# Kernel optimization log

Hardware: AMD Instinct MI355X
Metric: run time of the kernel (lower is better)

The kernel has to match this reference:

```python
import jax, jax.numpy as jnp
import numpy as np


def setup_inputs() -> dict:
    key = jax.random.key(0)
    kq, kk, kv = jax.random.split(key, 3)
    B, Q, K, D = 8, 2048, 2048, 1024
    return {
        "queries": jax.random.normal(kq, (B, Q, D), dtype=jnp.float32),
        "keys": jax.random.normal(kk, (B, K, D), dtype=jnp.float32),
        "values": jax.random.normal(kv, (B, K, D), dtype=jnp.float32),
    }


def reference(queries, keys, values):
    # scores: [B, Q, K] = queries @ keys^T
    scores = jnp.einsum("bqd,bkd->bqk", queries, keys)
    # NOTE: softmax over dim=1, i.e. the QUERY axis (non-standard)
    attn = jax.nn.softmax(scores, axis=1)
    # output: [B, Q, D]
    return jnp.einsum("bqk,bkd->bqd", attn, values)
```

## Files before the change

kernel.cpp:

```cpp
#include <hip/hip_runtime.h>
#include <stdint.h>

typedef _Float16 half8 __attribute__((ext_vector_type(8)));
typedef __attribute__((ext_vector_type(4))) float f32x4;
typedef __attribute__((ext_vector_type(8))) unsigned short us8;

__device__ inline unsigned short f2h(float x) {
  _Float16 h = (_Float16)x;
  return __builtin_bit_cast(unsigned short, h);
}

__device__ inline void ld16(const unsigned short* g, unsigned short* l) {
  __builtin_amdgcn_global_load_lds(
      (const __attribute__((address_space(1))) unsigned int*)g,
      (__attribute__((address_space(3))) unsigned int*)l, 16, 0, 0);
}

__global__ void k_cast16(const float* __restrict__ in, unsigned short* __restrict__ o, long n8) {
  long i = (long)blockIdx.x * blockDim.x + threadIdx.x;
  if (i >= n8) return;
  float4 a = ((const float4*)in)[i * 2];
  float4 b = ((const float4*)in)[i * 2 + 1];
  us8 h;
  h[0] = f2h(a.x); h[1] = f2h(a.y); h[2] = f2h(a.z); h[3] = f2h(a.w);
  h[4] = f2h(b.x); h[5] = f2h(b.y); h[6] = f2h(b.z); h[7] = f2h(b.w);
  *(us8*)(o + i * 8) = h;
}

__global__ void k_transpose16(const float* __restrict__ V, unsigned short* __restrict__ VT,
                              int Kn, int Dn) {
  __shared__ unsigned short t[64][65];
  const int b = blockIdx.z;
  const int k0 = blockIdx.x * 64, d0 = blockIdx.y * 64;
  const int c = threadIdx.x & 63, rr = threadIdx.x >> 6;
  const float* pV = V + (long)b * Kn * Dn;
  unsigned short* pT = VT + (long)b * Dn * Kn;
#pragma unroll
  for (int i = 0; i < 16; ++i) {
    int r = rr + i * 4;
    t[r][c] = f2h(pV[(long)(k0 + r) * Dn + d0 + c]);
  }
  __syncthreads();
#pragma unroll
  for (int i = 0; i < 16; ++i) {
    int r = rr + i * 4;
    pT[(long)(d0 + r) * Kn + k0 + c] = t[c][r];
  }
}


#define SBAR() __builtin_amdgcn_s_barrier()
#define SCHED0() __builtin_amdgcn_sched_barrier(0)
#define VMC(n) do { asm volatile("s_waitcnt vmcnt(" #n ")" ::: "memory"); } while (0)

template <int STATS>
__launch_bounds__(512, 2)
__global__ void k_gemm_bt(const unsigned short* __restrict__ A,
                          const unsigned short* __restrict__ B,
                          float* __restrict__ C, float2* __restrict__ ps,
                          int N, int Kin, long sA, long sB, long sC) {
  __shared__ unsigned short sAb[4][256 * 32];
  __shared__ unsigned short sBb[4][256 * 32];

  const int tid = threadIdx.x;
  const int lane = tid & 63, wave = tid >> 6;
  const int wr = wave >> 2, wc = wave & 3;
  const int l15 = lane & 15;

  const int nx = gridDim.x, ny = gridDim.y;
  int wg = ((int)blockIdx.z * ny + blockIdx.y) * nx + blockIdx.x;
  const int nwg = nx * ny * (int)gridDim.z;
  wg = (wg & 7) * (nwg >> 3) + (wg >> 3);
  const int tn = wg % nx, tm = (wg / nx) % ny, b = wg / (nx * ny);

  const unsigned short* pA = A + b * sA + (long)tm * 256 * Kin;
  const unsigned short* pB = B + b * sB + (long)tn * 256 * Kin;
  float* pC = C + b * sC;

  const int rlo = tid >> 2;
  const int csw = ((tid & 3) * 8) ^ (((rlo >> 1) & 3) << 3);
  const long ga = (long)rlo * Kin + csw;
  const long gh = (long)128 * Kin;

  const int ksw = ((lane >> 4) * 8) ^ (((l15 >> 1) & 3) << 3);
  const int aoff = (wr * 128 + l15) * 32 + ksw;
  const int boff = (wc * 64 + l15) * 32 + ksw;

#define STG(t, q) do { \
    ld16(pA + ga + (long)(t) * 32, &sAb[q][tid * 8]); \
    ld16(pA + ga + gh + (long)(t) * 32, &sAb[q][4096 + tid * 8]); \
    ld16(pB + ga + (long)(t) * 32, &sBb[q][tid * 8]); \
    ld16(pB + ga + gh + (long)(t) * 32, &sBb[q][4096 + tid * 8]); } while (0)

#define LDA8(q, m) (*(const half8*)&sAb[q][aoff + (m) * 512])
#define LDB8(q, n) (*(const half8*)&sBb[q][boff + (n) * 512])

  f32x4 acc[8][4];
#pragma unroll
  for (int i = 0; i < 8; ++i)
#pragma unroll
    for (int j = 0; j < 4; ++j)
#pragma unroll
      for (int r = 0; r < 4; ++r) acc[i][j][r] = 0.f;

  half8 aL[2][4], bC[2][4], aH[4];

#define READ_LO(s, q) \
  aL[s][0] = LDA8(q, 0); aL[s][1] = LDA8(q, 1); aL[s][2] = LDA8(q, 2); aL[s][3] = LDA8(q, 3); \
  bC[s][0] = LDB8(q, 0); bC[s][1] = LDB8(q, 1); bC[s][2] = LDB8(q, 2); bC[s][3] = LDB8(q, 3);

#define READ_HI(q) \
  aH[0] = LDA8(q, 4); aH[1] = LDA8(q, 5); aH[2] = LDA8(q, 6); aH[3] = LDA8(q, 7);

#define MFMA_ROW(m, a, s) \
  acc[m][0] = __builtin_amdgcn_mfma_f32_16x16x32_f16(a, bC[s][0], acc[m][0], 0, 0, 0); \
  acc[m][1] = __builtin_amdgcn_mfma_f32_16x16x32_f16(a, bC[s][1], acc[m][1], 0, 0, 0); \
  acc[m][2] = __builtin_amdgcn_mfma_f32_16x16x32_f16(a, bC[s][2], acc[m][2], 0, 0, 0); \
  acc[m][3] = __builtin_amdgcn_mfma_f32_16x16x32_f16(a, bC[s][3], acc[m][3], 0, 0, 0);

#define MFMA_LO(s) \
  __builtin_amdgcn_s_setprio(1); \
  MFMA_ROW(0, aL[s][0], s) MFMA_ROW(1, aL[s][1], s) \
  MFMA_ROW(2, aL[s][2], s) MFMA_ROW(3, aL[s][3], s) \
  __builtin_amdgcn_s_setprio(0);

#define MFMA_HI(s) \
  __builtin_amdgcn_s_setprio(1); \
  MFMA_ROW(4, aH[0], s) MFMA_ROW(5, aH[1], s) \
  MFMA_ROW(6, aH[2], s) MFMA_ROW(7, aH[3], s) \
  __builtin_amdgcn_s_setprio(0);

#define TILE_MAIN(t, s, sn) \
  READ_HI((t) & 3); \
  STG((t) + 2, ((t) + 2) & 3); \
  MFMA_LO(s) \
  VMC(4); SBAR(); SCHED0(); \
  READ_LO(sn, ((t) + 1) & 3); \
  MFMA_HI(s)

  const int nt = Kin >> 5;

  STG(0, 0);
  STG(1, 1);
  VMC(4); SBAR(); SCHED0();
  READ_LO(0, 0);

  for (int t = 0; t + 3 < nt; t += 2) {
    TILE_MAIN(t, 0, 1);
    TILE_MAIN(t + 1, 1, 0);
  }
  {
    READ_HI((nt - 2) & 3);
    MFMA_LO(0)
    VMC(0); SBAR(); SCHED0();
    READ_LO(1, (nt - 1) & 3);
    MFMA_HI(0)
    READ_HI((nt - 1) & 3);
    MFMA_LO(1)
    MFMA_HI(1)
  }

  const int crow0 = tm * 256 + wr * 128 + (lane >> 4) * 4;
  const int ccol0 = tn * 256 + wc * 64 + l15;
#pragma unroll
  for (int m = 0; m < 8; ++m)
#pragma unroll
    for (int n = 0; n < 4; ++n)
#pragma unroll
      for (int r = 0; r < 4; ++r)
        pC[(long)(crow0 + m * 16 + r) * N + ccol0 + n * 16] = acc[m][n][r];

  if constexpr (STATS) {
#pragma unroll
    for (int n = 0; n < 4; ++n) {
      float mx = -3.0e38f;
#pragma unroll
      for (int m = 0; m < 8; ++m)
#pragma unroll
        for (int r = 0; r < 4; ++r) mx = fmaxf(mx, acc[m][n][r]);
      mx = fmaxf(mx, __shfl_xor(mx, 16, 64));
      mx = fmaxf(mx, __shfl_xor(mx, 32, 64));
      float l = 0.f;
#pragma unroll
      for (int m = 0; m < 8; ++m)
#pragma unroll
        for (int r = 0; r < 4; ++r) l += __expf(acc[m][n][r] - mx);
      l += __shfl_xor(l, 16, 64);
      l += __shfl_xor(l, 32, 64);
      if (lane < 16) {
        int col = tn * 256 + wc * 64 + n * 16 + lane;
        ps[((long)(b * 16 + tm * 2 + wr)) * N + col] = make_float2(mx, l);
      }
    }
  }
}

__global__ void k_stats_combine(const float2* __restrict__ ps, float2* __restrict__ st, int Kn) {
  const long i = (long)blockIdx.x * blockDim.x + threadIdx.x;
  const int b = (int)(i / Kn), k = (int)(i % Kn);
  float M = -3.0e38f;
#pragma unroll
  for (int j = 0; j < 16; ++j) M = fmaxf(M, ps[((long)(b * 16 + j)) * Kn + k].x);
  float L = 0.f;
#pragma unroll
  for (int j = 0; j < 16; ++j) {
    float2 v = ps[((long)(b * 16 + j)) * Kn + k];
    L += v.y * __expf(v.x - M);
  }
  st[i] = make_float2(M, 1.0f / L);
}

__global__ void k_pcomp(const float* __restrict__ S, const float2* __restrict__ st,
                        unsigned short* __restrict__ P) {
  const long i = (long)blockIdx.x * blockDim.x + threadIdx.x;
  const long r = i >> 8;
  const int kb = (int)(i & 255) * 8;
  const int b = (int)(r >> 11);
  const float* sp = S + r * 2048 + kb;
  float4 s0 = *(const float4*)sp;
  float4 s1 = *(const float4*)(sp + 4);
  const float2* tp = st + (long)b * 2048 + kb;
  us8 o;
  float sv[8] = {s0.x, s0.y, s0.z, s0.w, s1.x, s1.y, s1.z, s1.w};
#pragma unroll
  for (int j = 0; j < 8; ++j) {
    float2 t = tp[j];
    o[j] = f2h(__expf(sv[j] - t.x) * t.y);
  }
  *(us8*)(P + r * 2048 + kb) = o;
}

extern "C" void kernel_launch(void* const* d_in, const int* in_sizes, int n_in,
                              void* d_out, int out_size, void* d_ws, size_t ws_size,
                              hipStream_t stream) {
  const float* Q = (const float*)d_in[0];
  const float* Kp = (const float*)d_in[1];
  const float* V = (const float*)d_in[2];
  float* out = (float*)d_out;

  constexpr int Bb = 8, Qn = 2048, Kn = 2048, Dn = 1024;
  constexpr long QD = (long)Qn * Dn, KD = (long)Kn * Dn, QK = (long)Qn * Kn, DK = (long)Dn * Kn;

  const size_t per = 3 * (size_t)(QD * 2)
                   + (size_t)(QK * 4)
                   + (size_t)(QK * 2)
                   + (size_t)(16 * Kn * 8)
                   + (size_t)(Kn * 8);
  int cb = 8;
  while (cb > 1 && (size_t)cb * per > ws_size) cb >>= 1;

  char* w = (char*)d_ws;
  unsigned short* q16 = (unsigned short*)w; w += (size_t)cb * QD * 2;
  unsigned short* k16 = (unsigned short*)w; w += (size_t)cb * KD * 2;
  unsigned short* vt  = (unsigned short*)w; w += (size_t)cb * DK * 2;
  float* S            = (float*)w;          w += (size_t)cb * QK * 4;
  unsigned short* P   = (unsigned short*)w; w += (size_t)cb * QK * 2;
  float2* ps          = (float2*)w;         w += (size_t)cb * 16 * Kn * 8;
  float2* st          = (float2*)w;

  for (int b0 = 0; b0 < Bb; b0 += cb) {
    int nb = (cb < Bb - b0) ? cb : (Bb - b0);
    long n8 = (long)nb * QD / 8;
    k_cast16<<<(int)(n8 / 256), 256, 0, stream>>>(Q + b0 * QD, q16, n8);
    k_cast16<<<(int)(n8 / 256), 256, 0, stream>>>(Kp + b0 * KD, k16, n8);
    k_transpose16<<<dim3(Kn / 64, Dn / 64, nb), 256, 0, stream>>>(V + b0 * KD, vt, Kn, Dn);
    k_gemm_bt<1><<<dim3(Kn / 256, Qn / 256, nb), 512, 0, stream>>>(
        q16, k16, S, ps, Kn, Dn, QD, KD, QK);
    k_stats_combine<<<nb * Kn / 256, 256, 0, stream>>>(ps, st, Kn);
    k_pcomp<<<(int)((long)nb * QK / 8 / 256), 256, 0, stream>>>(S, st, P);
    k_gemm_bt<0><<<dim3(Dn / 256, Qn / 256, nb), 512, 0, stream>>>(
        P, vt, out + b0 * QD, nullptr, Dn, Kn, QK, DK, QD);
  }
}
```

Baseline: 411.5 us.

## Fuse fp16 casts and softmax normalization into GEMM loads, chunk over keys

Removes the separate Q/K cast kernels and the P computation kernel. The first GEMM now loads fp32 Q/K through registers, converts them to fp16 and writes them to LDS. The second GEMM reads fp32 scores and applies exp-normalization on the fly. Key dimension is split into chunks with output accumulation, so the workspace shrinks and all batches run in one launch. This trades async global-to-LDS copies for register-staged loads with conversion ALU work, and adds read-modify-write passes over the output.

```diff
diff --git a/kernel.cpp b/kernel.cpp
--- a/kernel.cpp
+++ b/kernel.cpp
@@ -16,49 +16,40 @@
       (__attribute__((address_space(3))) unsigned int*)l, 16, 0, 0);
 }
 
-__global__ void k_cast16(const float* __restrict__ in, unsigned short* __restrict__ o, long n8) {
-  long i = (long)blockIdx.x * blockDim.x + threadIdx.x;
-  if (i >= n8) return;
-  float4 a = ((const float4*)in)[i * 2];
-  float4 b = ((const float4*)in)[i * 2 + 1];
-  us8 h;
-  h[0] = f2h(a.x); h[1] = f2h(a.y); h[2] = f2h(a.z); h[3] = f2h(a.w);
-  h[4] = f2h(b.x); h[5] = f2h(b.y); h[6] = f2h(b.z); h[7] = f2h(b.w);
-  *(us8*)(o + i * 8) = h;
-}
-
 __global__ void k_transpose16(const float* __restrict__ V, unsigned short* __restrict__ VT,
-                              int Kn, int Dn) {
+                              int Kn, int Dn, int k0c, int Kc) {
   __shared__ unsigned short t[64][65];
   const int b = blockIdx.z;
   const int k0 = blockIdx.x * 64, d0 = blockIdx.y * 64;
   const int c = threadIdx.x & 63, rr = threadIdx.x >> 6;
   const float* pV = V + (long)b * Kn * Dn;
-  unsigned short* pT = VT + (long)b * Dn * Kn;
+  unsigned short* pT = VT + (long)b * Dn * Kc;
 #pragma unroll
   for (int i = 0; i < 16; ++i) {
     int r = rr + i * 4;
-    t[r][c] = f2h(pV[(long)(k0 + r) * Dn + d0 + c]);
+    t[r][c] = f2h(pV[(long)(k0c + k0 + r) * Dn + d0 + c]);
   }
   __syncthreads();
 #pragma unroll
   for (int i = 0; i < 16; ++i) {
     int r = rr + i * 4;
-    pT[(long)(d0 + r) * Kn + k0 + c] = t[c][r];
+    pT[(long)(d0 + r) * Kc + k0 + c] = t[c][r];
   }
 }
 
 
 #define SBAR() __builtin_amdgcn_s_barrier()
 #define SCHED0() __builtin_amdgcn_sched_barrier(0)
-#define VMC(n) do { asm volatile("s_waitcnt vmcnt(" #n ")" ::: "memory"); } while (0)
-
-template <int STATS>
+#define LGKM0() asm volatile("s_waitcnt lgkmcnt(0)" ::: "memory")
+
+template <int MODE, int ACC>
 __launch_bounds__(512, 2)
-__global__ void k_gemm_bt(const unsigned short* __restrict__ A,
-                          const unsigned short* __restrict__ B,
-                          float* __restrict__ C, float2* __restrict__ ps,
-                          int N, int Kin, long sA, long sB, long sC) {
+__global__ void k_gemm(const float* __restrict__ Af,
+                       const float* __restrict__ Bf,
+                       const unsigned short* __restrict__ Bh,
+                       const float2* __restrict__ st,
+                       float* __restrict__ C, float2* __restrict__ ps,
+                       int N, int Kin, long sA, long sB, long sC) {
   __shared__ unsigned short sAb[4][256 * 32];
   __shared__ unsigned short sBb[4][256 * 32];
 
@@ -73,28 +64,91 @@
   wg = (wg & 7) * (nwg >> 3) + (wg >> 3);
   const int tn = wg % nx, tm = (wg / nx) % ny, b = wg / (nx * ny);
 
-  const unsigned short* pA = A + b * sA + (long)tm * 256 * Kin;
-  const unsigned short* pB = B + b * sB + (long)tn * 256 * Kin;
+  const float* pA = Af + b * sA + (long)tm * 256 * Kin;
+  const float* pBf = nullptr;
+  const unsigned short* pBh = nullptr;
+  const float2* stp = nullptr;
+  if constexpr (MODE == 0) pBf = Bf + b * sB + (long)tn * 256 * Kin;
+  else { pBh = Bh + b * sB + (long)tn * 256 * Kin; stp = st + (long)b * Kin; }
   float* pC = C + b * sC;
 
   const int rlo = tid >> 2;
-  const int csw = ((tid & 3) * 8) ^ (((rlo >> 1) & 3) << 3);
-  const long ga = (long)rlo * Kin + csw;
-  const long gh = (long)128 * Kin;
+  const int c0 = (tid & 3) * 8;
+  const int key = ((rlo >> 1) & 3) << 3;
+  const int cx = c0 ^ key;
+  const long arA = (long)rlo * Kin + c0;
+  const long arA2 = arA + 128L * Kin;
+  const long gaB = (long)rlo * Kin + cx;
+  const long ghB = 128L * Kin;
 
   const int ksw = ((lane >> 4) * 8) ^ (((l15 >> 1) & 3) << 3);
   const int aoff = (wr * 128 + l15) * 32 + ksw;
   const int boff = (wc * 64 + l15) * 32 + ksw;
 
-#define STG(t, q) do { \
-    ld16(pA + ga + (long)(t) * 32, &sAb[q][tid * 8]); \
-    ld16(pA + ga + gh + (long)(t) * 32, &sAb[q][4096 + tid * 8]); \
-    ld16(pB + ga + (long)(t) * 32, &sBb[q][tid * 8]); \
-    ld16(pB + ga + gh + (long)(t) * 32, &sBb[q][4096 + tid * 8]); } while (0)
-
 #define LDA8(q, m) (*(const half8*)&sAb[q][aoff + (m) * 512])
 #define LDB8(q, n) (*(const half8*)&sBb[q][boff + (n) * 512])
 
+  float4 La0, La1, La2, La3, Lb0, Lb1, Lb2, Lb3;
+
+#define ISSUE(t) do { \
+    const long kb_ = (long)(t) * 32; \
+    if constexpr (MODE == 1) { \
+      ld16(pBh + gaB + kb_, &sBb[(t) & 3][tid * 8]); \
+      ld16(pBh + gaB + ghB + kb_, &sBb[(t) & 3][4096 + tid * 8]); \
+    } \
+    La0 = *(const float4*)(pA + arA + kb_); \
+    La1 = *(const float4*)(pA + arA + kb_ + 4); \
+    La2 = *(const float4*)(pA + arA2 + kb_); \
+    La3 = *(const float4*)(pA + arA2 + kb_ + 4); \
+    if constexpr (MODE == 0) { \
+      Lb0 = *(const float4*)(pBf + arA + kb_); \
+      Lb1 = *(const float4*)(pBf + arA + kb_ + 4); \
+      Lb2 = *(const float4*)(pBf + arA2 + kb_); \
+      Lb3 = *(const float4*)(pBf + arA2 + kb_ + 4); \
+    } else { \
+      const float2* sp_ = stp + kb_ + c0; \
+      Lb0 = *(const float4*)sp_;       Lb1 = *(const float4*)(sp_ + 2); \
+      Lb2 = *(const float4*)(sp_ + 4); Lb3 = *(const float4*)(sp_ + 6); \
+    } \
+  } while (0)
+
+#define CVTW(q) do { \
+    us8 h_; \
+    if constexpr (MODE == 0) { \
+      h_[0]=f2h(La0.x); h_[1]=f2h(La0.y); h_[2]=f2h(La0.z); h_[3]=f2h(La0.w); \
+      h_[4]=f2h(La1.x); h_[5]=f2h(La1.y); h_[6]=f2h(La1.z); h_[7]=f2h(La1.w); \
+      *(us8*)&sAb[q][rlo * 32 + cx] = h_; \
+      h_[0]=f2h(La2.x); h_[1]=f2h(La2.y); h_[2]=f2h(La2.z); h_[3]=f2h(La2.w); \
+      h_[4]=f2h(La3.x); h_[5]=f2h(La3.y); h_[6]=f2h(La3.z); h_[7]=f2h(La3.w); \
+      *(us8*)&sAb[q][4096 + rlo * 32 + cx] = h_; \
+      h_[0]=f2h(Lb0.x); h_[1]=f2h(Lb0.y); h_[2]=f2h(Lb0.z); h_[3]=f2h(Lb0.w); \
+      h_[4]=f2h(Lb1.x); h_[5]=f2h(Lb1.y); h_[6]=f2h(Lb1.z); h_[7]=f2h(Lb1.w); \
+      *(us8*)&sBb[q][rlo * 32 + cx] = h_; \
+      h_[0]=f2h(Lb2.x); h_[1]=f2h(Lb2.y); h_[2]=f2h(Lb2.z); h_[3]=f2h(Lb2.w); \
+      h_[4]=f2h(Lb3.x); h_[5]=f2h(Lb3.y); h_[6]=f2h(Lb3.z); h_[7]=f2h(Lb3.w); \
+      *(us8*)&sBb[q][4096 + rlo * 32 + cx] = h_; \
+    } else { \
+      h_[0]=f2h(__expf(La0.x - Lb0.x) * Lb0.y); \
+      h_[1]=f2h(__expf(La0.y - Lb0.z) * Lb0.w); \
+      h_[2]=f2h(__expf(La0.z - Lb1.x) * Lb1.y); \
+      h_[3]=f2h(__expf(La0.w - Lb1.z) * Lb1.w); \
+      h_[4]=f2h(__expf(La1.x - Lb2.x) * Lb2.y); \
+      h_[5]=f2h(__expf(La1.y - Lb2.z) * Lb2.w); \
+      h_[6]=f2h(__expf(La1.z - Lb3.x) * Lb3.y); \
+      h_[7]=f2h(__expf(La1.w - Lb3.z) * Lb3.w); \
+      *(us8*)&sAb[q][rlo * 32 + cx] = h_; \
+      h_[0]=f2h(__expf(La2.x - Lb0.x) * Lb0.y); \
+      h_[1]=f2h(__expf(La2.y - Lb0.z) * Lb0.w); \
+      h_[2]=f2h(__expf(La2.z - Lb1.x) * Lb1.y); \
+      h_[3]=f2h(__expf(La2.w - Lb1.z) * Lb1.w); \
+      h_[4]=f2h(__expf(La3.x - Lb2.x) * Lb2.y); \
+      h_[5]=f2h(__expf(La3.y - Lb2.z) * Lb2.w); \
+      h_[6]=f2h(__expf(La3.z - Lb3.x) * Lb3.y); \
+      h_[7]=f2h(__expf(La3.w - Lb3.z) * Lb3.w); \
+      *(us8*)&sAb[q][4096 + rlo * 32 + cx] = h_; \
+    } \
+  } while (0)
+
   f32x4 acc[8][4];
 #pragma unroll
   for (int i = 0; i < 8; ++i)
@@ -103,10 +157,10 @@
 #pragma unroll
       for (int r = 0; r < 4; ++r) acc[i][j][r] = 0.f;
 
-  half8 aL[2][4], bC[2][4], aH[4];
+  half8 aL[4], bC[2][4], aH[4];
 
 #define READ_LO(s, q) \
-  aL[s][0] = LDA8(q, 0); aL[s][1] = LDA8(q, 1); aL[s][2] = LDA8(q, 2); aL[s][3] = LDA8(q, 3); \
+  aL[0] = LDA8(q, 0); aL[1] = LDA8(q, 1); aL[2] = LDA8(q, 2); aL[3] = LDA8(q, 3); \
   bC[s][0] = LDB8(q, 0); bC[s][1] = LDB8(q, 1); bC[s][2] = LDB8(q, 2); bC[s][3] = LDB8(q, 3);
 
 #define READ_HI(q) \
@@ -120,8 +174,8 @@
 
 #define MFMA_LO(s) \
   __builtin_amdgcn_s_setprio(1); \
-  MFMA_ROW(0, aL[s][0], s) MFMA_ROW(1, aL[s][1], s) \
-  MFMA_ROW(2, aL[s][2], s) MFMA_ROW(3, aL[s][3], s) \
+  MFMA_ROW(0, aL[0], s) MFMA_ROW(1, aL[1], s) \
+  MFMA_ROW(2, aL[2], s) MFMA_ROW(3, aL[3], s) \
   __builtin_amdgcn_s_setprio(0);
 
 #define MFMA_HI(s) \
@@ -130,29 +184,29 @@
   MFMA_ROW(6, aH[2], s) MFMA_ROW(7, aH[3], s) \
   __builtin_amdgcn_s_setprio(0);
 
-#define TILE_MAIN(t, s, sn) \
+#define TILE(t, s, sn) \
+  ISSUE((t) + 2); SCHED0(); \
   READ_HI((t) & 3); \
-  STG((t) + 2, ((t) + 2) & 3); \
   MFMA_LO(s) \
-  VMC(4); SBAR(); SCHED0(); \
+  CVTW(((t) + 2) & 3); \
+  SCHED0(); LGKM0(); SBAR(); SCHED0(); \
   READ_LO(sn, ((t) + 1) & 3); \
   MFMA_HI(s)
 
   const int nt = Kin >> 5;
 
-  STG(0, 0);
-  STG(1, 1);
-  VMC(4); SBAR(); SCHED0();
+  ISSUE(0); CVTW(0);
+  ISSUE(1); CVTW(1);
+  LGKM0(); SBAR(); SCHED0();
   READ_LO(0, 0);
 
   for (int t = 0; t + 3 < nt; t += 2) {
-    TILE_MAIN(t, 0, 1);
-    TILE_MAIN(t + 1, 1, 0);
+    TILE(t, 0, 1);
+    TILE(t + 1, 1, 0);
   }
   {
     READ_HI((nt - 2) & 3);
     MFMA_LO(0)
-    VMC(0); SBAR(); SCHED0();
     READ_LO(1, (nt - 1) & 3);
     MFMA_HI(0)
     READ_HI((nt - 1) & 3);
@@ -167,10 +221,13 @@
 #pragma unroll
     for (int n = 0; n < 4; ++n)
 #pragma unroll
-      for (int r = 0; r < 4; ++r)
-        pC[(long)(crow0 + m * 16 + r) * N + ccol0 + n * 16] = acc[m][n][r];
-
-  if constexpr (STATS) {
+      for (int r = 0; r < 4; ++r) {
+        long idx = (long)(crow0 + m * 16 + r) * N + ccol0 + n * 16;
+        if constexpr (ACC) pC[idx] += acc[m][n][r];
+        else pC[idx] = acc[m][n][r];
+      }
+
+  if constexpr (MODE == 0) {
 #pragma unroll
     for (int n = 0; n < 4; ++n) {
       float mx = -3.0e38f;
@@ -195,39 +252,19 @@
   }
 }
 
-__global__ void k_stats_combine(const float2* __restrict__ ps, float2* __restrict__ st, int Kn) {
+__global__ void k_stats_combine(const float2* __restrict__ ps, float2* __restrict__ st, int Kc) {
   const long i = (long)blockIdx.x * blockDim.x + threadIdx.x;
-  const int b = (int)(i / Kn), k = (int)(i % Kn);
+  const int b = (int)(i / Kc), k = (int)(i % Kc);
   float M = -3.0e38f;
 #pragma unroll
-  for (int j = 0; j < 16; ++j) M = fmaxf(M, ps[((long)(b * 16 + j)) * Kn + k].x);
+  for (int j = 0; j < 16; ++j) M = fmaxf(M, ps[((long)(b * 16 + j)) * Kc + k].x);
   float L = 0.f;
 #pragma unroll
   for (int j = 0; j < 16; ++j) {
-    float2 v = ps[((long)(b * 16 + j)) * Kn + k];
+    float2 v = ps[((long)(b * 16 + j)) * Kc + k];
     L += v.y * __expf(v.x - M);
   }
   st[i] = make_float2(M, 1.0f / L);
-}
-
-__global__ void k_pcomp(const float* __restrict__ S, const float2* __restrict__ st,
-                        unsigned short* __restrict__ P) {
-  const long i = (long)blockIdx.x * blockDim.x + threadIdx.x;
-  const long r = i >> 8;
-  const int kb = (int)(i & 255) * 8;
-  const int b = (int)(r >> 11);
-  const float* sp = S + r * 2048 + kb;
-  float4 s0 = *(const float4*)sp;
-  float4 s1 = *(const float4*)(sp + 4);
-  const float2* tp = st + (long)b * 2048 + kb;
-  us8 o;
-  float sv[8] = {s0.x, s0.y, s0.z, s0.w, s1.x, s1.y, s1.z, s1.w};
-#pragma unroll
-  for (int j = 0; j < 8; ++j) {
-    float2 t = tp[j];
-    o[j] = f2h(__expf(sv[j] - t.x) * t.y);
-  }
-  *(us8*)(P + r * 2048 + kb) = o;
 }
 
 extern "C" void kernel_launch(void* const* d_in, const int* in_sizes, int n_in,
@@ -239,36 +276,39 @@
   float* out = (float*)d_out;
 
   constexpr int Bb = 8, Qn = 2048, Kn = 2048, Dn = 1024;
-  constexpr long QD = (long)Qn * Dn, KD = (long)Kn * Dn, QK = (long)Qn * Kn, DK = (long)Dn * Kn;
-
-  const size_t per = 3 * (size_t)(QD * 2)
-                   + (size_t)(QK * 4)
-                   + (size_t)(QK * 2)
-                   + (size_t)(16 * Kn * 8)
-                   + (size_t)(Kn * 8);
-  int cb = 8;
-  while (cb > 1 && (size_t)cb * per > ws_size) cb >>= 1;
+  constexpr long QD = (long)Qn * Dn, KD = (long)Kn * Dn;
+
+  long Kc = 1024;
+  {
+    size_t need = (size_t)Bb * Qn * Kc * 4
+                + (size_t)Bb * Dn * Kc * 2
+                + (size_t)Bb * 16 * Kc * 8
+                + (size_t)Bb * Kc * 8;
+    if (need > ws_size) Kc = 512;
+  }
+  const int nc = Kn / (int)Kc;
 
   char* w = (char*)d_ws;
-  unsigned short* q16 = (unsigned short*)w; w += (size_t)cb * QD * 2;
-  unsigned short* k16 = (unsigned short*)w; w += (size_t)cb * KD * 2;
-  unsigned short* vt  = (unsigned short*)w; w += (size_t)cb * DK * 2;
-  float* S            = (float*)w;          w += (size_t)cb * QK * 4;
-  unsigned short* P   = (unsigned short*)w; w += (size_t)cb * QK * 2;
-  float2* ps          = (float2*)w;         w += (size_t)cb * 16 * Kn * 8;
-  float2* st          = (float2*)w;
-
-  for (int b0 = 0; b0 < Bb; b0 += cb) {
-    int nb = (cb < Bb - b0) ? cb : (Bb - b0);
-    long n8 = (long)nb * QD / 8;
-    k_cast16<<<(int)(n8 / 256), 256, 0, stream>>>(Q + b0 * QD, q16, n8);
-    k_cast16<<<(int)(n8 / 256), 256, 0, stream>>>(Kp + b0 * KD, k16, n8);
-    k_transpose16<<<dim3(Kn / 64, Dn / 64, nb), 256, 0, stream>>>(V + b0 * KD, vt, Kn, Dn);
-    k_gemm_bt<1><<<dim3(Kn / 256, Qn / 256, nb), 512, 0, stream>>>(
-        q16, k16, S, ps, Kn, Dn, QD, KD, QK);
-    k_stats_combine<<<nb * Kn / 256, 256, 0, stream>>>(ps, st, Kn);
-    k_pcomp<<<(int)((long)nb * QK / 8 / 256), 256, 0, stream>>>(S, st, P);
-    k_gemm_bt<0><<<dim3(Dn / 256, Qn / 256, nb), 512, 0, stream>>>(
-        P, vt, out + b0 * QD, nullptr, Dn, Kn, QK, DK, QD);
-  }
-}
+  float* S           = (float*)w;          w += (size_t)Bb * Qn * Kc * 4;
+  unsigned short* vt = (unsigned short*)w; w += (size_t)Bb * Dn * Kc * 2;
+  float2* ps         = (float2*)w;         w += (size_t)Bb * 16 * Kc * 8;
+  float2* st         = (float2*)w;
+
+  for (int c = 0; c < nc; ++c) {
+    const int k0c = c * (int)Kc;
+    k_transpose16<<<dim3((int)Kc / 64, Dn / 64, Bb), 256, 0, stream>>>(
+        V, vt, Kn, Dn, k0c, (int)Kc);
+    k_gemm<0, 0><<<dim3((int)Kc / 256, Qn / 256, Bb), 512, 0, stream>>>(
+        Q, Kp + (long)k0c * Dn, nullptr, nullptr, S, ps,
+        (int)Kc, Dn, QD, KD, (long)Qn * Kc);
+    k_stats_combine<<<Bb * (int)Kc / 256, 256, 0, stream>>>(ps, st, (int)Kc);
+    if (c == 0)
+      k_gemm<1, 0><<<dim3(Dn / 256, Qn / 256, Bb), 512, 0, stream>>>(
+          S, nullptr, vt, st, out, nullptr, Dn, (int)Kc,
+          (long)Qn * Kc, (long)Dn * Kc, QD);
+    else
+      k_gemm<1, 1><<<dim3(Dn / 256, Qn / 256, Bb), 512, 0, stream>>>(
+          S, nullptr, vt, st, out, nullptr, Dn, (int)Kc,
+          (long)Qn * Kc, (long)Dn * Kc, QD);
+  }
+}
```

New measurement: 496.6 us. 1.21x slower.

## Chunk attention over key axis across all batches and accumulate output

Applied to the files above, without the earlier changes.

The launcher used to loop over batch chunks sized to fit the workspace. It now processes all 8 batches at once and splits the key axis into chunks, starting at 1024 columns. This works because the softmax runs over the query axis, so each key column can be normalised on its own. The second GEMM gains an accumulate mode so later chunks add into the output, and the K-cast buffer is reused to hold P, shrinking the workspace and the score buffer. In exchange there are extra kernel launches, a read-modify-write pass over the output for each added chunk, and smaller grids for the score GEMM.

```diff
diff --git a/kernel.cpp b/kernel.cpp
--- a/kernel.cpp
+++ b/kernel.cpp
@@ -27,24 +27,39 @@
   *(us8*)(o + i * 8) = h;
 }
 
+__global__ void k_cast16c(const float* __restrict__ in, unsigned short* __restrict__ o,
+                          int Kn, int Dn, int k0c, int Kc) {
+  const long i = (long)blockIdx.x * blockDim.x + threadIdx.x;
+  const long cols8 = (long)Kc * Dn / 8;
+  const int b = (int)(i / cols8);
+  const long j = i - (long)b * cols8;
+  const float* p = in + (long)b * Kn * Dn + (long)k0c * Dn + j * 8;
+  float4 a = *(const float4*)p;
+  float4 c = *(const float4*)(p + 4);
+  us8 h;
+  h[0] = f2h(a.x); h[1] = f2h(a.y); h[2] = f2h(a.z); h[3] = f2h(a.w);
+  h[4] = f2h(c.x); h[5] = f2h(c.y); h[6] = f2h(c.z); h[7] = f2h(c.w);
+  *(us8*)(o + (long)b * Kc * Dn + j * 8) = h;
+}
+
 __global__ void k_transpose16(const float* __restrict__ V, unsigned short* __restrict__ VT,
-                              int Kn, int Dn) {
+                              int Kn, int Dn, int k0c, int Kc) {
   __shared__ unsigned short t[64][65];
   const int b = blockIdx.z;
   const int k0 = blockIdx.x * 64, d0 = blockIdx.y * 64;
   const int c = threadIdx.x & 63, rr = threadIdx.x >> 6;
   const float* pV = V + (long)b * Kn * Dn;
-  unsigned short* pT = VT + (long)b * Dn * Kn;
+  unsigned short* pT = VT + (long)b * Dn * Kc;
 #pragma unroll
   for (int i = 0; i < 16; ++i) {
     int r = rr + i * 4;
-    t[r][c] = f2h(pV[(long)(k0 + r) * Dn + d0 + c]);
+    t[r][c] = f2h(pV[(long)(k0c + k0 + r) * Dn + d0 + c]);
   }
   __syncthreads();
 #pragma unroll
   for (int i = 0; i < 16; ++i) {
     int r = rr + i * 4;
-    pT[(long)(d0 + r) * Kn + k0 + c] = t[c][r];
+    pT[(long)(d0 + r) * Kc + k0 + c] = t[c][r];
   }
 }
 
@@ -53,7 +68,7 @@
 #define SCHED0() __builtin_amdgcn_sched_barrier(0)
 #define VMC(n) do { asm volatile("s_waitcnt vmcnt(" #n ")" ::: "memory"); } while (0)
 
-template <int STATS>
+template <int STATS, int ACC>
 __launch_bounds__(512, 2)
 __global__ void k_gemm_bt(const unsigned short* __restrict__ A,
                           const unsigned short* __restrict__ B,
@@ -167,8 +182,11 @@
 #pragma unroll
     for (int n = 0; n < 4; ++n)
 #pragma unroll
-      for (int r = 0; r < 4; ++r)
-        pC[(long)(crow0 + m * 16 + r) * N + ccol0 + n * 16] = acc[m][n][r];
+      for (int r = 0; r < 4; ++r) {
+        long idx = (long)(crow0 + m * 16 + r) * N + ccol0 + n * 16;
+        if constexpr (ACC) pC[idx] += acc[m][n][r];
+        else pC[idx] = acc[m][n][r];
+      }
 
   if constexpr (STATS) {
 #pragma unroll
@@ -195,31 +213,32 @@
   }
 }
 
-__global__ void k_stats_combine(const float2* __restrict__ ps, float2* __restrict__ st, int Kn) {
+__global__ void k_stats_combine(const float2* __restrict__ ps, float2* __restrict__ st, int Kc) {
   const long i = (long)blockIdx.x * blockDim.x + threadIdx.x;
-  const int b = (int)(i / Kn), k = (int)(i % Kn);
+  const int b = (int)(i / Kc), k = (int)(i % Kc);
   float M = -3.0e38f;
 #pragma unroll
-  for (int j = 0; j < 16; ++j) M = fmaxf(M, ps[((long)(b * 16 + j)) * Kn + k].x);
+  for (int j = 0; j < 16; ++j) M = fmaxf(M, ps[((long)(b * 16 + j)) * Kc + k].x);
   float L = 0.f;
 #pragma unroll
   for (int j = 0; j < 16; ++j) {
-    float2 v = ps[((long)(b * 16 + j)) * Kn + k];
+    float2 v = ps[((long)(b * 16 + j)) * Kc + k];
     L += v.y * __expf(v.x - M);
   }
   st[i] = make_float2(M, 1.0f / L);
 }
 
 __global__ void k_pcomp(const float* __restrict__ S, const float2* __restrict__ st,
-                        unsigned short* __restrict__ P) {
+                        unsigned short* __restrict__ P, int Kc) {
   const long i = (long)blockIdx.x * blockDim.x + threadIdx.x;
-  const long r = i >> 8;
-  const int kb = (int)(i & 255) * 8;
+  const int kw = Kc >> 3;
+  const long r = i / kw;
+  const int kb = (int)(i - r * kw) * 8;
   const int b = (int)(r >> 11);
-  const float* sp = S + r * 2048 + kb;
+  const float* sp = S + r * Kc + kb;
   float4 s0 = *(const float4*)sp;
   float4 s1 = *(const float4*)(sp + 4);
-  const float2* tp = st + (long)b * 2048 + kb;
+  const float2* tp = st + (long)b * Kc + kb;
   us8 o;
   float sv[8] = {s0.x, s0.y, s0.z, s0.w, s1.x, s1.y, s1.z, s1.w};
 #pragma unroll
@@ -227,7 +246,7 @@
     float2 t = tp[j];
     o[j] = f2h(__expf(sv[j] - t.x) * t.y);
   }
-  *(us8*)(P + r * 2048 + kb) = o;
+  *(us8*)(P + r * Kc + kb) = o;
 }
 
 extern "C" void kernel_launch(void* const* d_in, const int* in_sizes, int n_in,
@@ -239,36 +258,51 @@
   float* out = (float*)d_out;
 
   constexpr int Bb = 8, Qn = 2048, Kn = 2048, Dn = 1024;
-  constexpr long QD = (long)Qn * Dn, KD = (long)Kn * Dn, QK = (long)Qn * Kn, DK = (long)Dn * Kn;
-
-  const size_t per = 3 * (size_t)(QD * 2)
-                   + (size_t)(QK * 4)
-                   + (size_t)(QK * 2)
-                   + (size_t)(16 * Kn * 8)
-                   + (size_t)(Kn * 8);
-  int cb = 8;
-  while (cb > 1 && (size_t)cb * per > ws_size) cb >>= 1;
+  constexpr long QD = (long)Qn * Dn;
+
+  long Kc = 1024;
+  for (;;) {
+    size_t uKP = (size_t)Bb * Qn * Kc * 2;
+    size_t need = (size_t)Bb * QD * 2
+                + uKP
+                + (size_t)Bb * Dn * Kc * 2
+                + (size_t)Bb * Qn * Kc * 4
+                + (size_t)Bb * 16 * Kc * 8
+                + (size_t)Bb * Kc * 8;
+    if (need <= ws_size || Kc == 256) break;
+    Kc >>= 1;
+  }
+  const int nc = Kn / (int)Kc;
 
   char* w = (char*)d_ws;
-  unsigned short* q16 = (unsigned short*)w; w += (size_t)cb * QD * 2;
-  unsigned short* k16 = (unsigned short*)w; w += (size_t)cb * KD * 2;
-  unsigned short* vt  = (unsigned short*)w; w += (size_t)cb * DK * 2;
-  float* S            = (float*)w;          w += (size_t)cb * QK * 4;
-  unsigned short* P   = (unsigned short*)w; w += (size_t)cb * QK * 2;
-  float2* ps          = (float2*)w;         w += (size_t)cb * 16 * Kn * 8;
+  unsigned short* q16 = (unsigned short*)w; w += (size_t)Bb * QD * 2;
+  unsigned short* kp  = (unsigned short*)w; w += (size_t)Bb * Qn * Kc * 2;
+  unsigned short* vt  = (unsigned short*)w; w += (size_t)Bb * Dn * Kc * 2;
+  float* S            = (float*)w;          w += (size_t)Bb * Qn * Kc * 4;
+  float2* ps          = (float2*)w;         w += (size_t)Bb * 16 * Kc * 8;
   float2* st          = (float2*)w;
 
-  for (int b0 = 0; b0 < Bb; b0 += cb) {
-    int nb = (cb < Bb - b0) ? cb : (Bb - b0);
-    long n8 = (long)nb * QD / 8;
-    k_cast16<<<(int)(n8 / 256), 256, 0, stream>>>(Q + b0 * QD, q16, n8);
-    k_cast16<<<(int)(n8 / 256), 256, 0, stream>>>(Kp + b0 * KD, k16, n8);
-    k_transpose16<<<dim3(Kn / 64, Dn / 64, nb), 256, 0, stream>>>(V + b0 * KD, vt, Kn, Dn);
-    k_gemm_bt<1><<<dim3(Kn / 256, Qn / 256, nb), 512, 0, stream>>>(
-        q16, k16, S, ps, Kn, Dn, QD, KD, QK);
-    k_stats_combine<<<nb * Kn / 256, 256, 0, stream>>>(ps, st, Kn);
-    k_pcomp<<<(int)((long)nb * QK / 8 / 256), 256, 0, stream>>>(S, st, P);
-    k_gemm_bt<0><<<dim3(Dn / 256, Qn / 256, nb), 512, 0, stream>>>(
-        P, vt, out + b0 * QD, nullptr, Dn, Kn, QK, DK, QD);
-  }
-}
+  unsigned short* k16c = kp;
+  unsigned short* P    = kp;
+
+  k_cast16<<<(int)(Bb * QD / 8 / 256), 256, 0, stream>>>(Q, q16, Bb * QD / 8);
+
+  for (int c = 0; c < nc; ++c) {
+    const int k0c = c * (int)Kc;
+    k_cast16c<<<(int)((long)Bb * Kc * Dn / 8 / 256), 256, 0, stream>>>(
+        Kp, k16c, Kn, Dn, k0c, (int)Kc);
+    k_transpose16<<<dim3((int)Kc / 64, Dn / 64, Bb), 256, 0, stream>>>(
+        V, vt, Kn, Dn, k0c, (int)Kc);
+    k_gemm_bt<1, 0><<<dim3((int)Kc / 256, Qn / 256, Bb), 512, 0, stream>>>(
+        q16, k16c, S, ps, (int)Kc, Dn, QD, (long)Kc * Dn, (long)Qn * Kc);
+    k_stats_combine<<<Bb * (int)Kc / 256, 256, 0, stream>>>(ps, st, (int)Kc);
+    k_pcomp<<<(int)((long)Bb * Qn * (Kc / 8) / 256), 256, 0, stream>>>(
+        S, st, P, (int)Kc);
+    if (c == 0)
+      k_gemm_bt<0, 0><<<dim3(Dn / 256, Qn / 256, Bb), 512, 0, stream>>>(
+          P, vt, out, nullptr, Dn, (int)Kc, (long)Qn * Kc, (long)Dn * Kc, QD);
+    else
+      k_gemm_bt<0, 1><<<dim3(Dn / 256, Qn / 256, Bb), 512, 0, stream>>>(
+          P, vt, out, nullptr, Dn, (int)Kc, (long)Qn * Kc, (long)Dn * Kc, QD);
+  }
+}
```

New measurement: 454.5 us. 1.1x slower.
